# Optimization experiments

Measured on AMD Instinct MI355X. Metric: run time of the kernel, lower is better.

## Reference

```python
import jax, jax.numpy as jnp
import numpy as np

N = 50000      # nodes
E = 800000     # edges (avg degree 16)
F_IN = 256     # input feature dim
H, D = 4, 32   # heads, per-head dim
HD = H * D
K = 25000      # SAGPool keeps ceil(0.5*N) nodes
C = 2          # classes
SLOPE = 0.4
NEG = -1e9

def _gat(x, src, dst, valid, n, W, b, al, ar):
    # DGL GATConv: fc -> per-head attn logits -> edge softmax over dst -> weighted sum
    h = (x @ W).reshape(-1, H, D)                      # [n,H,D]
    el = jnp.einsum('nhd,hd->nh', h, al)
    er = jnp.einsum('nhd,hd->nh', h, ar)
    e = jax.nn.leaky_relu(el[src] + er[dst], SLOPE)    # [E,H]
    e = jnp.where(valid[:, None], e, NEG)
    m = jnp.maximum(jax.ops.segment_max(e, dst, num_segments=n), NEG)
    ex = jnp.exp(e - m[dst]) * valid[:, None].astype(x.dtype)
    s = jax.ops.segment_sum(ex, dst, num_segments=n)
    alpha = ex / jnp.maximum(s[dst], 1e-16)            # [E,H] edge softmax
    out = jax.ops.segment_sum(alpha[:, :, None] * h[src], dst, num_segments=n)
    return out + b.reshape(1, H, D), alpha

def _sagpool(x, src, dst, valid, n, k, Wc, bc):
    # score = GraphConv(in,1) with symmetric norm; keep top-k nodes, scale by tanh(score)
    vf = valid.astype(x.dtype)
    deg_o = jnp.maximum(jax.ops.segment_sum(vf, src, num_segments=n), 1.0)
    deg_i = jnp.maximum(jax.ops.segment_sum(vf, dst, num_segments=n), 1.0)
    h = (x @ Wc) * (deg_o ** -0.5)[:, None]
    agg = jax.ops.segment_sum(h[src] * vf[:, None], dst, num_segments=n)
    score = (agg * (deg_i ** -0.5)[:, None] + bc)[:, 0]   # [n]
    vals, perm = jax.lax.top_k(score, k)
    xk = x[perm] * jnp.tanh(vals)[:, None]                # [k,F]
    new_id = jnp.full((n,), -1, jnp.int32).at[perm].set(jnp.arange(k, dtype=jnp.int32))
    ns, nd = new_id[src], new_id[dst]
    nv = valid & (ns >= 0) & (nd >= 0)                    # edges fully inside subgraph
    return xk, jnp.where(nv, ns, 0), jnp.where(nv, nd, 0), nv

def setup_inputs():
    key = jax.random.key(0)
    k = jax.random.split(key, 18)
    rn = lambda i, shape, scale: jax.random.normal(k[i], shape, jnp.float32) * scale
    return {
        "feature": rn(0, (N, F_IN), 1.0),
        "strength": jax.random.uniform(k[1], (E,), dtype=jnp.float32),
        "W0": rn(2, (F_IN, HD), F_IN ** -0.5), "b0": jnp.zeros((HD,), jnp.float32),
        "al0": rn(3, (H, D), 0.1), "ar0": rn(4, (H, D), 0.1),
        "Wc0": rn(5, (HD, 1), HD ** -0.5), "bc0": jnp.zeros((1,), jnp.float32),
        "W1": rn(6, (HD, HD), HD ** -0.5), "b1": jnp.zeros((HD,), jnp.float32),
        "al1": rn(7, (H, D), 0.1), "ar1": rn(8, (H, D), 0.1),
        "gate_W": rn(9, (D, 1), D ** -0.5), "gate_b": jnp.zeros((1,), jnp.float32),
        "cls_W": rn(10, (D, C), D ** -0.5), "cls_b": jnp.zeros((C,), jnp.float32),
        "src": jax.random.randint(k[11], (E,), 0, N, dtype=jnp.int32),
        "dst": jax.random.randint(k[12], (E,), 0, N, dtype=jnp.int32),
    }

def reference(feature, strength, W0, b0, al0, ar0, Wc0, bc0, W1, b1, al1, ar1,
              gate_W, gate_b, cls_W, cls_b, src, dst):
    valid0 = jnp.ones((E,), bool)
    h0, _ = _gat(feature, src, dst, valid0, N, W0, b0, al0, ar0)
    x = h0.reshape(N, HD)                                  # flatten(1)
    x1, s1, d1, v1 = _sagpool(x, src, dst, valid0, N, K, Wc0, bc0)
    h1, atten = _gat(x1, s1, d1, v1, K, W1, b1, al1, ar1)  # get_attention=True
    strength1 = strength * v1.astype(strength.dtype)       # edata carried into subgraph (masked)
    res = h1.mean(axis=1)                                  # [K,D] mean over heads
    gate = jax.nn.softmax(res @ gate_W + gate_b, axis=0)   # [K,1] GlobalAttentionPooling
    readout = jnp.sum(gate * res, axis=0, keepdims=True)   # [1,D]
    lbl_pred = readout @ cls_W + cls_b                     # [1,C]
    return (readout, lbl_pred, atten, strength1)
```

## Files before the change

### kernel.cpp

```cpp
#include <hip/hip_runtime.h>
#include <stdint.h>

#define NN 50000
#define EE 800000
#define FIN 256
#define HD 128
#define DD 32
#define KK 25000
#define SLOPEF 0.4f
#define NEGF (-1e9f)
#define ATT_OFF 34
#define STR_OFF (34 + EE * 4)
#define CW 128

#define BCH 32
#define EPC (EE / BCH)

__device__ __forceinline__ unsigned fkey(float x) {
    unsigned u = __float_as_uint(x);
    return (u & 0x80000000u) ? ~u : (u | 0x80000000u);
}
__device__ __forceinline__ float unfkey(unsigned k) {
    unsigned u = (k & 0x80000000u) ? (k ^ 0x80000000u) : ~k;
    return __uint_as_float(u);
}
__device__ __forceinline__ float lrelu(float v) { return v > 0.f ? v : SLOPEF * v; }

struct P {
    const float *feature, *strength, *W0, *b0, *al0, *ar0, *Wc0, *bc0;
    const float *W1, *b1, *al1, *ar1, *gW, *gb, *cW, *cb;
    const int *src, *dst;
    double *Zacc, *racc;
    int *cnt;
    unsigned *gmaxk, *rs;
    unsigned *binsHi, *binsLo;
    unsigned *keys;
    unsigned char *degc_i, *degc_o, *degc1;
    unsigned *cb0, *cb1;
    int *dsum;
    int *ens, *end_;
    int *csr_src, *rank, *off0, *off1, *sel, *slot, *list, *bsum, *boff;
    float *z0, *el0, *er0, *q4, *m0f, *s0f, *b0wc, *hc, *score, *xk, *z1;
    float *el1, *er1, *m1f, *s1f, *res, *g, *tscale;
    float *out;
};

#define BM 128
#define BN 64
#define BK 16
__device__ void gemm_body(
    const float* __restrict__ A, const float* __restrict__ B, float* __restrict__ C,
    int M, int Kd,
    const float* __restrict__ al, const float* __restrict__ ar,
    float* __restrict__ el, float* __restrict__ er,
    const float* __restrict__ Wc, float* __restrict__ q4,
    int bx, int by) {
    __shared__ float As[BK][BM + 4];
    __shared__ float Bs[BK][BN];
    int bm = by * BM, bn = bx * BN;
    int tid = threadIdx.x;
    int tr = tid >> 4, tc = tid & 15;
    int lrow = tid >> 1;
    int arow = (bm + lrow < M) ? (bm + lrow) : -1;
    float acc[8][4] = {};
    for (int k0 = 0; k0 < Kd; k0 += BK) {
        {
            int col = (tid & 1) << 3;
            float4 v0 = {0.f,0.f,0.f,0.f}, v1 = {0.f,0.f,0.f,0.f};
            if (arow >= 0) {
                const float* ap = A + (size_t)arow * Kd + k0 + col;
                v0 = *(const float4*)ap; v1 = *(const float4*)(ap + 4);
            }
            As[col + 0][lrow] = v0.x; As[col + 1][lrow] = v0.y;
            As[col + 2][lrow] = v0.z; As[col + 3][lrow] = v0.w;
            As[col + 4][lrow] = v1.x; As[col + 5][lrow] = v1.y;
            As[col + 6][lrow] = v1.z; As[col + 7][lrow] = v1.w;
        }
        {
            int kr = tid >> 4, col = (tid & 15) << 2;
            float4 v = *(const float4*)(B + (size_t)(k0 + kr) * HD + bn + col);
            *(float4*)&Bs[kr][col] = v;
        }
        __syncthreads();
#pragma unroll
        for (int kk = 0; kk < BK; kk++) {
            float a[8], b[4];
#pragma unroll
            for (int i = 0; i < 8; i++) a[i] = As[kk][tr * 8 + i];
#pragma unroll
            for (int j = 0; j < 4; j++) b[j] = Bs[kk][tc * 4 + j];
#pragma unroll
            for (int i = 0; i < 8; i++)
#pragma unroll
                for (int j = 0; j < 4; j++) acc[i][j] = fmaf(a[i], b[j], acc[i][j]);
        }
        __syncthreads();
    }
#pragma unroll
    for (int i = 0; i < 8; i++) {
        int gr = bm + tr * 8 + i;
        if (gr < M) {
            float4 v = {acc[i][0], acc[i][1], acc[i][2], acc[i][3]};
            *(float4*)(C + (size_t)gr * HD + bn + tc * 4) = v;
        }
    }
    int head = bx * 2 + (tc >> 3);
    int dbase = (tc & 7) * 4;
    const float* alh = al + head * 32 + dbase;
    const float* arh = ar + head * 32 + dbase;
    float a0 = alh[0], a1 = alh[1], a2 = alh[2], a3 = alh[3];
    float r0 = arh[0], r1 = arh[1], r2 = arh[2], r3 = arh[3];
    float w0 = 0.f, w1 = 0.f, w2 = 0.f, w3 = 0.f;
    if (Wc) {
        const float* wch = Wc + head * 32 + dbase;
        w0 = wch[0]; w1 = wch[1]; w2 = wch[2]; w3 = wch[3];
    }
#pragma unroll
    for (int i = 0; i < 8; i++) {
        int gr = bm + tr * 8 + i;
        float pe = acc[i][0]*a0 + acc[i][1]*a1 + acc[i][2]*a2 + acc[i][3]*a3;
        float pr = acc[i][0]*r0 + acc[i][1]*r1 + acc[i][2]*r2 + acc[i][3]*r3;
        float pq = acc[i][0]*w0 + acc[i][1]*w1 + acc[i][2]*w2 + acc[i][3]*w3;
#pragma unroll
        for (int o = 1; o < 8; o <<= 1) {
            pe += __shfl_xor(pe, o); pr += __shfl_xor(pr, o); pq += __shfl_xor(pq, o);
        }
        if ((tc & 7) == 0 && gr < M) {
            el[gr * 4 + head] = pe; er[gr * 4 + head] = pr;
            if (Wc) q4[gr * 4 + head] = pq;
        }
    }
}

__global__ __launch_bounds__(256) void k_count0(P p) {
    __shared__ unsigned hist[NN / 4];
    int blk = blockIdx.x;
    int isD = blk < BCH;
    int c = isD ? blk : blk - BCH;
    for (int w = threadIdx.x; w < NN / 4; w += 256) hist[w] = 0u;
    __syncthreads();
    int j0 = c * EPC, j1 = j0 + EPC;
    if (isD) {
        for (int e = j0 + (int)threadIdx.x; e < j1; e += 256) {
            int d = p.dst[e];
            unsigned sh = (unsigned)(d & 3) * 8u;
            unsigned old = atomicAdd(&hist[d >> 2], 1u << sh);
            p.rank[e] = (int)((old >> sh) & 0xffu);
        }
    } else {
        for (int e = j0 + (int)threadIdx.x; e < j1; e += 256) {
            int s = p.src[e];
            atomicAdd(&hist[s >> 2], 1u << ((unsigned)(s & 3) * 8u));
        }
    }
    __syncthreads();
    unsigned* o32 = (unsigned*)((isD ? p.degc_i : p.degc_o) + (size_t)c * NN);
    for (int w = threadIdx.x; w < NN / 4; w += 256) o32[w] = hist[w];
}

__global__ __launch_bounds__(256) void k_count1(P p) {
    __shared__ unsigned hist[KK / 4];
    int c = blockIdx.x;
    for (int w = threadIdx.x; w < KK / 4; w += 256) hist[w] = 0u;
    __syncthreads();
    int j0 = c * EPC, j1 = j0 + EPC;
    for (int e = j0 + (int)threadIdx.x; e < j1; e += 256) {
        int d = p.end_[e];
        if (d >= 0) {
            unsigned sh = (unsigned)(d & 3) * 8u;
            unsigned old = atomicAdd(&hist[d >> 2], 1u << sh);
            p.rank[e] = (int)((old >> sh) & 0xffu);
        }
    }
    __syncthreads();
    unsigned* o32 = (unsigned*)(p.degc1 + (size_t)c * KK);
    for (int w = threadIdx.x; w < KK / 4; w += 256) o32[w] = hist[w];
}

__global__ void k_emap(P p) {
    int e = blockIdx.x * blockDim.x + threadIdx.x;
    if (e >= EE) return;
    int ns = p.slot[p.src[e]], nd = p.slot[p.dst[e]];
    if (ns < 0) nd = -1;
    p.ens[e] = ns;
    p.end_[e] = nd;
}

__global__ __launch_bounds__(256) void k_bsum(const unsigned char* __restrict__ deg,
                                              int* __restrict__ bsum, int n, int nn) {
    int i = blockIdx.x * 256 + threadIdx.x;
    int v = 0;
    if (i < n) {
#pragma unroll
        for (int c = 0; c < BCH; c++) v += deg[(size_t)c * nn + i];
    }
    int lane = threadIdx.x & 63, w = threadIdx.x >> 6;
    __shared__ int ws[4];
#pragma unroll
    for (int o = 1; o < 64; o <<= 1) v += __shfl_xor(v, o);
    if (lane == 0) ws[w] = v;
    __syncthreads();
    if (threadIdx.x == 0) bsum[blockIdx.x] = ws[0] + ws[1] + ws[2] + ws[3];
}
__global__ __launch_bounds__(256) void k_bscan(const int* __restrict__ bsum, int nb,
                                               int* __restrict__ boff,
                                               int* __restrict__ off, int n) {
    __shared__ int ws[4];
    __shared__ int wo[5];
    int t = threadIdx.x;
    int v = (t < nb) ? bsum[t] : 0;
    int lane = t & 63, w = t >> 6;
    int incl = v;
    for (int o = 1; o < 64; o <<= 1) { int u = __shfl_up(incl, o); if (lane >= o) incl += u; }
    if (lane == 63) ws[w] = incl;
    __syncthreads();
    if (t == 0) { int a = 0; for (int i = 0; i < 4; i++) { wo[i] = a; a += ws[i]; } wo[4] = a; }
    __syncthreads();
    if (t < nb) boff[t] = wo[w] + incl - v;
    if (t == 0) off[n] = wo[4];
}
__global__ __launch_bounds__(256) void k_fscan0(P p) {
    __shared__ int ws[4];
    __shared__ int wo[4];
    int i = blockIdx.x * 256 + threadIdx.x;
    int v = 0;
    if (i < NN) {
#pragma unroll
        for (int c = 0; c < BCH; c++) v += p.degc_i[(size_t)c * NN + i];
    }
    int lane = threadIdx.x & 63, w = threadIdx.x >> 6;
    int incl = v;
    for (int o = 1; o < 64; o <<= 1) { int u = __shfl_up(incl, o); if (lane >= o) incl += u; }
    if (lane == 63) ws[w] = incl;
    __syncthreads();
    if (threadIdx.x == 0) { int a = 0; for (int k = 0; k < 4; k++) { wo[k] = a; a += ws[k]; } }
    __syncthreads();
    if (i < NN) {
        int base = p.boff[blockIdx.x] + wo[w] + incl - v;
        p.off0[i] = base;
        unsigned run = (unsigned)base;
        int s = 0;
#pragma unroll
        for (int c = 0; c < BCH; c++) {
            p.cb0[(size_t)c * NN + i] = run;
            run += p.degc_i[(size_t)c * NN + i];
            s += p.degc_o[(size_t)c * NN + i];
        }
        p.dsum[i] = s;
    }
}
__global__ __launch_bounds__(256) void k_fscan1(P p) {
    __shared__ int ws[4];
    __shared__ int wo[4];
    int i = blockIdx.x * 256 + threadIdx.x;
    int v = 0;
    if (i < KK) {
#pragma unroll
        for (int c = 0; c < BCH; c++) v += p.degc1[(size_t)c * KK + i];
    }
    int lane = threadIdx.x & 63, w = threadIdx.x >> 6;
    int incl = v;
    for (int o = 1; o < 64; o <<= 1) { int u = __shfl_up(incl, o); if (lane >= o) incl += u; }
    if (lane == 63) ws[w] = incl;
    __syncthreads();
    if (threadIdx.x == 0) { int a = 0; for (int k = 0; k < 4; k++) { wo[k] = a; a += ws[k]; } }
    __syncthreads();
    if (i < KK) {
        int base = p.boff[blockIdx.x] + wo[w] + incl - v;
        p.off1[i] = base;
        unsigned run = (unsigned)base;
#pragma unroll
        for (int c = 0; c < BCH; c++) {
            p.cb1[(size_t)c * KK + i] = run;
            run += p.degc1[(size_t)c * KK + i];
        }
    }
}

#define G0B 782
#define GB_E 3125
__global__ __launch_bounds__(256) void k_g0sc(P p) {
    int blk = blockIdx.x;
    if (blk < G0B) {
        gemm_body(p.feature, p.W0, p.z0, NN, FIN, p.al0, p.ar0, p.el0, p.er0,
                  p.Wc0, p.q4, blk & 1, blk >> 1);
    } else if (blk < G0B + GB_E) {
        int e = (blk - G0B) * 256 + threadIdx.x;
        if (e < EE) {
            int c = e / EPC;
            int d = p.dst[e];
            unsigned pos = p.cb0[(size_t)c * NN + d] + (unsigned)p.rank[e];
            p.csr_src[pos] = p.src[e];
        }
    } else {
        int l = threadIdx.x;
        if (l < 64) {
            float t = p.b0[l] * p.Wc0[l] + p.b0[l + 64] * p.Wc0[l + 64];
#pragma unroll
            for (int o = 1; o < 64; o <<= 1) t += __shfl_xor(t, o);
            if (l == 0) p.b0wc[0] = t;
        }
    }
}

#define G1B 392
__global__ __launch_bounds__(256) void k_g1sc(P p) {
    int blk = blockIdx.x;
    if (blk < G1B) {
        gemm_body(p.xk, p.W1, p.z1, KK, HD, p.al1, p.ar1, p.el1, p.er1,
                  nullptr, nullptr, blk & 1, blk >> 1);
    } else {
        int e = (blk - G1B) * 256 + threadIdx.x;
        if (e < EE) {
            int d = p.end_[e];
            if (d >= 0) {
                int c = e / EPC;
                unsigned pos = p.cb1[(size_t)c * KK + d] + (unsigned)p.rank[e];
                p.csr_src[pos] = p.ens[e];
            }
        }
    }
}

__global__ __launch_bounds__(256) void k_fgatlite(
    const int* __restrict__ off, const int* __restrict__ csrs,
    const float* __restrict__ el, const float* __restrict__ er,
    const float* __restrict__ q4, const int* __restrict__ dsum,
    const float* __restrict__ b0wc,
    float* __restrict__ hc, float* __restrict__ m0f, float* __restrict__ s0f) {
    int wv = threadIdx.x >> 6, lane = threadIdx.x & 63;
    int v = blockIdx.x * 4 + wv;
    int b = off[v], e = off[v + 1], deg = e - b;
    int h = lane >> 4, sub = lane & 15;
    float erh = er[(size_t)v * 4 + h];
    float m = NEGF;
    for (int li = sub; li < deg; li += 16) {
        int s = csrs[b + li];
        m = fmaxf(m, lrelu(el[(size_t)s * 4 + h] + erh));
    }
#pragma unroll
    for (int o = 1; o < 16; o <<= 1) m = fmaxf(m, __shfl_xor(m, o));
    float ssum = 0.f, hq = 0.f;
    for (int li = sub; li < deg; li += 16) {
        int s = csrs[b + li];
        float ex = expf(lrelu(el[(size_t)s * 4 + h] + erh) - m);
        ssum += ex;
        hq = fmaf(ex, q4[(size_t)s * 4 + h], hq);
    }
#pragma unroll
    for (int o = 1; o < 16; o <<= 1) { ssum += __shfl_xor(ssum, o); hq += __shfl_xor(hq, o); }
    if (sub == 0) { m0f[v * 4 + h] = m; s0f[v * 4 + h] = ssum; }
    float t = hq / fmaxf(ssum, 1e-16f);
    t += __shfl_xor(t, 16);
    t += __shfl_xor(t, 32);
    if (lane == 0)
        hc[v] = (t + b0wc[0]) / sqrtf(fmaxf((float)dsum[v], 1.f));
}

__global__ __launch_bounds__(256) void k_fgatx(
    const int* __restrict__ list, const float* __restrict__ tscale,
    const int* __restrict__ off, const int* __restrict__ csrs,
    const float* __restrict__ el, const float* __restrict__ er,
    const float* __restrict__ m0f, const float* __restrict__ s0f,
    const float* __restrict__ z, const float* __restrict__ b0,
    float* __restrict__ xk) {
    __shared__ int ssrc[4][CW];
    __shared__ float sexp[4][CW][4];
    int wv = threadIdx.x >> 6, lane = threadIdx.x & 63;
    int i = blockIdx.x * 4 + wv;
    int v = list[i];
    int b = off[v], e = off[v + 1], deg = e - b;
    int h = lane >> 4, sub = lane & 15;
    float erh = er[(size_t)v * 4 + h];
    float mh = m0f[v * 4 + h];
    for (int li = sub; li < deg; li += 16) {
        int s = csrs[b + li];
        if (h == 0 && li < CW) ssrc[wv][li] = s;
        if (li < CW) sexp[wv][li][h] = expf(lrelu(el[(size_t)s * 4 + h] + erh) - mh);
    }
    __syncthreads();
    int h0 = lane >> 5, h1 = h0 + 2;
    float s0 = s0f[v * 4 + h0], s1 = s0f[v * 4 + h1];
    float m0 = m0f[v * 4 + h0], m1 = m0f[v * 4 + h1];
    float er0v = er[(size_t)v * 4 + h0], er1v = er[(size_t)v * 4 + h1];
    int c0 = lane, c1 = lane + 64;
    float acc0 = 0.f, acc1 = 0.f;
    for (int li = 0; li < deg; li++) {
        int s; float w0, w1;
        if (li < CW) {
            s = ssrc[wv][li];
            w0 = sexp[wv][li][h0]; w1 = sexp[wv][li][h1];
        } else {
            s = csrs[b + li];
            w0 = expf(lrelu(el[(size_t)s * 4 + h0] + er0v) - m0);
            w1 = expf(lrelu(el[(size_t)s * 4 + h1] + er1v) - m1);
        }
        int su = __builtin_amdgcn_readfirstlane(s);
        const float* zr = z + (size_t)su * HD;
        acc0 = fmaf(w0, zr[c0], acc0);
        acc1 = fmaf(w1, zr[c1], acc1);
    }
    float ts = tscale[i];
    float* xr = xk + (size_t)i * HD;
    xr[c0] = (acc0 / fmaxf(s0, 1e-16f) + b0[c0]) * ts;
    xr[c1] = (acc1 / fmaxf(s1, 1e-16f) + b0[c1]) * ts;
}

__global__ void k_score(P p) {
    int v = blockIdx.x * blockDim.x + threadIdx.x;
    if (v >= NN) return;
    int b = p.off0[v], en = p.off0[v + 1];
    float acc = 0.f;
    for (int i = b; i < en; i++) acc += p.hc[p.csr_src[i]];
    float dg = fmaxf((float)(en - b), 1.f);
    float sc = acc / sqrtf(dg) + p.bc0[0];
    p.score[v] = sc;
    p.keys[v] = fkey(sc);
}

__global__ void k_hist2(P p, int level) {
    int v = blockIdx.x * blockDim.x + threadIdx.x;
    if (v >= NN) return;
    unsigned key = p.keys[v];
    if (level == 0) atomicAdd(&p.binsHi[key >> 16], 1u);
    else if ((key >> 16) == p.rs[2]) atomicAdd(&p.binsLo[key & 0xFFFFu], 1u);
}
__global__ __launch_bounds__(1024) void k_rsel2(P p, int level) {
    const unsigned* bins = level ? p.binsLo : p.binsHi;
    int K = level ? (int)p.rs[3] : KK;
    __shared__ unsigned wsm[16];
    __shared__ unsigned wpre[17];
    int t = threadIdx.x;
    unsigned base = (unsigned)t * 64;
    const uint4* b4 = (const uint4*)(bins + base);
    unsigned S = 0;
#pragma unroll
    for (int i = 0; i < 16; i++) {
        uint4 u = b4[i];
        S += u.x + u.y + u.z + u.w;
    }
    int lane = t & 63, w = t >> 6;
    unsigned val = S;
    for (int o = 1; o < 64; o <<= 1) { unsigned u = __shfl_up(val, o); if (lane >= o) val += u; }
    if (lane == 63) wsm[w] = val;
    __syncthreads();
    if (t == 0) { unsigned a = 0; for (int i = 0; i < 16; i++) { wpre[i] = a; a += wsm[i]; } wpre[16] = a; }
    __syncthreads();
    unsigned incl = wpre[w] + val;
    unsigned running = wpre[16] - incl;
    for (int i = 63; i >= 0; i--) {
        unsigned c = bins[base + i];
        unsigned above = running;
        running += c;
        if ((int)above < K && (int)running >= K) {
            if (level == 0) { p.rs[2] = base + (unsigned)i; p.rs[3] = (unsigned)(K - (int)above); }
            else { p.rs[0] = (p.rs[2] << 16) | (base + (unsigned)i); p.rs[1] = (unsigned)(K - (int)above); }
        }
    }
}
__global__ void k_sel(P p) {
    int v = blockIdx.x * blockDim.x + threadIdx.x;
    if (v >= NN) return;
    p.sel[v] = (p.keys[v] > p.rs[0]) ? 1 : 0;
}
__global__ __launch_bounds__(1024) void k_ties(P p) {
    __shared__ int base;
    __shared__ int wsums[16];
    unsigned pivot = p.rs[0];
    int need = (int)p.rs[1];
    if (threadIdx.x == 0) base = 0;
    __syncthreads();
    for (int st = 0; st < NN; st += 1024) {
        int v = st + (int)threadIdx.x;
        int flag = (v < NN && p.keys[v] == pivot) ? 1 : 0;
        unsigned long long m = __ballot(flag);
        int lane = threadIdx.x & 63, w = threadIdx.x >> 6;
        int pre = __popcll(m & ((1ull << lane) - 1ull));
        if (lane == 0) wsums[w] = __popcll(m);
        __syncthreads();
        int woff = 0;
        for (int i = 0; i < w; i++) woff += wsums[i];
        int rank = base + woff + pre;
        if (flag && rank < need) p.sel[v] = 1;
        __syncthreads();
        if (threadIdx.x == 0) {
            int s = 0;
            for (int i = 0; i < 16; i++) s += wsums[i];
            base += s;
        }
        __syncthreads();
    }
}
__global__ void k_list(P p) {
    int v = blockIdx.x * blockDim.x + threadIdx.x;
    if (v >= NN) return;
    if (p.sel[v]) {
        int i = atomicAdd(p.cnt, 1);
        p.list[i] = v;
        p.slot[v] = i;
        p.tscale[i] = tanhf(p.score[v]);
    } else {
        p.slot[v] = -1;
    }
}

__global__ __launch_bounds__(256) void k_fgat2(
    const int* __restrict__ off, const int* __restrict__ csrs,
    const float* __restrict__ el, const float* __restrict__ er,
    const float* __restrict__ z, const float* __restrict__ bias,
    float* __restrict__ mf, float* __restrict__ sf,
    const float* __restrict__ gW, const float* __restrict__ gb,
    float* __restrict__ res, float* __restrict__ g) {
    __shared__ int ssrc[4][CW];
    __shared__ float sexp[4][CW][4];
    int wv = threadIdx.x >> 6, lane = threadIdx.x & 63;
    int v = blockIdx.x * 4 + wv;
    int b = off[v], e = off[v + 1], deg = e - b;
    int h = lane >> 4, sub = lane & 15;
    float4 er4 = *(const float4*)(er + (size_t)v * 4);
    float erh = ((const float*)&er4)[h];
    float m = NEGF;
    for (int li = sub; li < deg; li += 16) {
        int s = csrs[b + li];
        if (h == 0 && li < CW) ssrc[wv][li] = s;
        m = fmaxf(m, lrelu(el[(size_t)s * 4 + h] + erh));
    }
#pragma unroll
    for (int o = 1; o < 16; o <<= 1) m = fmaxf(m, __shfl_xor(m, o));
    float ssum = 0.f;
    for (int li = sub; li < deg; li += 16) {
        int s = csrs[b + li];
        float x = expf(lrelu(el[(size_t)s * 4 + h] + erh) - m);
        if (li < CW) sexp[wv][li][h] = x;
        ssum += x;
    }
#pragma unroll
    for (int o = 1; o < 16; o <<= 1) ssum += __shfl_xor(ssum, o);
    if (sub == 0) { mf[v * 4 + h] = m; sf[v * 4 + h] = ssum; }
    __syncthreads();
    int h0 = lane >> 5, h1 = h0 + 2;
    float m0 = __shfl(m, h0 << 4), m1 = __shfl(m, h1 << 4);
    float s0 = __shfl(ssum, h0 << 4), s1 = __shfl(ssum, h1 << 4);
    int c0 = lane, c1 = lane + 64;
    float acc0 = 0.f, acc1 = 0.f;
    for (int li = 0; li < deg; li++) {
        int s; float w0, w1;
        if (li < CW) {
            s = ssrc[wv][li];
            w0 = sexp[wv][li][h0]; w1 = sexp[wv][li][h1];
        } else {
            s = csrs[b + li];
            w0 = expf(lrelu(el[(size_t)s * 4 + h0] + ((const float*)&er4)[h0]) - m0);
            w1 = expf(lrelu(el[(size_t)s * 4 + h1] + ((const float*)&er4)[h1]) - m1);
        }
        int su = __builtin_amdgcn_readfirstlane(s);
        const float* zr = z + (size_t)su * HD;
        acc0 = fmaf(w0, zr[c0], acc0);
        acc1 = fmaf(w1, zr[c1], acc1);
    }
    float xc0 = acc0 / fmaxf(s0, 1e-16f) + bias[c0];
    float xc1 = acc1 / fmaxf(s1, 1e-16f) + bias[c1];
    float t = xc0 + xc1;
    t += __shfl_xor(t, 32);
    float pg = 0.f;
    if (lane < 32) {
        float r = 0.25f * t;
        res[(size_t)v * 32 + lane] = r;
        pg = r * gW[lane];
    }
#pragma unroll
    for (int o = 1; o < 32; o <<= 1) pg += __shfl_xor(pg, o);
    if (lane == 0) g[v] = pg + gb[0];
}

__global__ void k_ealpha1(P p) {
    int e = blockIdx.x * blockDim.x + threadIdx.x;
    if (e >= EE) return;
    int ds = p.ens[e], dd = p.end_[e];
    float a[4] = {0.f, 0.f, 0.f, 0.f};
    float st = 0.f;
    if (dd >= 0) {
        float4 es = *(const float4*)(p.el1 + ds * 4);
        float4 ed = *(const float4*)(p.er1 + dd * 4);
        float l[4] = {lrelu(es.x + ed.x), lrelu(es.y + ed.y), lrelu(es.z + ed.z), lrelu(es.w + ed.w)};
#pragma unroll
        for (int h = 0; h < 4; h++) {
            float m = p.m1f[dd * 4 + h];
            float ex = expf(l[h] - m);
            a[h] = ex / fmaxf(p.s1f[dd * 4 + h], 1e-16f);
        }
        st = p.strength[e];
    }
    float* o = p.out + ATT_OFF + (size_t)e * 4;
    *(float2*)(o) = make_float2(a[0], a[1]);
    *(float2*)(o + 2) = make_float2(a[2], a[3]);
    p.out[STR_OFF + e] = st;
}

__global__ void k_gmax(P p) {
    __shared__ float red[256];
    int t = threadIdx.x;
    float m = -3.4e38f;
    for (int i = blockIdx.x * 256 + t; i < KK; i += gridDim.x * 256) m = fmaxf(m, p.g[i]);
    red[t] = m;
    __syncthreads();
    for (int o = 128; o > 0; o >>= 1) { if (t < o) red[t] = fmaxf(red[t], red[t + o]); __syncthreads(); }
    if (t == 0) atomicMax(p.gmaxk, fkey(red[0]));
}
#define WSUM_BLOCKS 104
__global__ __launch_bounds__(256) void k_wsum(P p) {
    __shared__ double vred[256];
    __shared__ double zred[8];
    int t = threadIdx.x, il = t >> 5, d = t & 31;
    float gm = unfkey(*p.gmaxk);
    double accv = 0.0, accw = 0.0;
    for (int i = blockIdx.x * 8 + il; i < KK; i += WSUM_BLOCKS * 8) {
        float w = expf(p.g[i] - gm);
        accv += (double)(w * p.res[(size_t)i * 32 + d]);
        if (d == 0) accw += (double)w;
    }
    vred[t] = accv;
    if (d == 0) zred[il] = accw;
    __syncthreads();
    if (il == 0) {
        double s = 0;
#pragma unroll
        for (int k2 = 0; k2 < 8; k2++) s += vred[k2 * 32 + d];
        atomicAdd(&p.racc[d], s);
    }
    if (t == 32) {
        double z2 = 0;
#pragma unroll
        for (int k2 = 0; k2 < 8; k2++) z2 += zred[k2];
        atomicAdd(p.Zacc, z2);
    }
}
__global__ void k_final(P p) {
    __shared__ float rb[32];
    int t = threadIdx.x;
    double Z = *p.Zacc;
    if (t < 32) {
        float r = (float)(p.racc[t] / Z);
        p.out[t] = r;
        rb[t] = r;
    }
    __syncthreads();
    if (t < 2) {
        float s = 0.f;
        for (int d = 0; d < 32; d++) s += rb[d] * p.cW[d * 2 + t];
        p.out[32 + t] = s + p.cb[t];
    }
}

extern "C" void kernel_launch(void* const* d_in, const int* in_sizes, int n_in,
                              void* d_out, int out_size, void* d_ws, size_t ws_size,
                              hipStream_t stream) {
    (void)in_sizes; (void)n_in; (void)out_size; (void)ws_size;
    P p;
    p.feature  = (const float*)d_in[0];
    p.strength = (const float*)d_in[1];
    p.W0  = (const float*)d_in[2];  p.b0  = (const float*)d_in[3];
    p.al0 = (const float*)d_in[4];  p.ar0 = (const float*)d_in[5];
    p.Wc0 = (const float*)d_in[6];  p.bc0 = (const float*)d_in[7];
    p.W1  = (const float*)d_in[8];  p.b1  = (const float*)d_in[9];
    p.al1 = (const float*)d_in[10]; p.ar1 = (const float*)d_in[11];
    p.gW  = (const float*)d_in[12]; p.gb  = (const float*)d_in[13];
    p.cW  = (const float*)d_in[14]; p.cb  = (const float*)d_in[15];
    p.src = (const int*)d_in[16];   p.dst = (const int*)d_in[17];
    p.out = (float*)d_out;

    char* ws = (char*)d_ws;
    size_t off = 0;
    auto alloc = [&](size_t bytes) -> void* {
        void* r = ws + off;
        off = (off + bytes + 255) & ~(size_t)255;
        return r;
    };
    p.Zacc  = (double*)alloc(8);
    p.racc  = (double*)alloc(32 * 8);
    p.cnt   = (int*)alloc(4);
    p.gmaxk = (unsigned*)alloc(4);
    p.rs    = (unsigned*)alloc(16);
    p.binsHi = (unsigned*)alloc(65536 * 4);
    p.binsLo = (unsigned*)alloc(65536 * 4);
    size_t zbytes = off;
    p.degc_i = (unsigned char*)alloc((size_t)BCH * NN);
    p.degc_o = (unsigned char*)alloc((size_t)BCH * NN);
    p.degc1  = p.degc_i;
    p.cb0 = (unsigned*)alloc((size_t)BCH * NN * 4);
    p.cb1 = p.cb0;
    p.dsum = (int*)alloc((size_t)NN * 4);
    p.ens  = (int*)alloc((size_t)EE * 4);
    p.end_ = (int*)alloc((size_t)EE * 4);
    p.z0 = (float*)alloc((size_t)NN * HD * 4);
    p.xk = (float*)alloc((size_t)KK * HD * 4);
    p.z1 = (float*)alloc((size_t)KK * HD * 4);
    p.csr_src = (int*)alloc((size_t)EE * 4);
    p.rank    = (int*)alloc((size_t)EE * 4);
    p.el0 = (float*)alloc((size_t)NN * 4 * 4);
    p.er0 = (float*)alloc((size_t)NN * 4 * 4);
    p.q4  = (float*)alloc((size_t)NN * 4 * 4);
    p.m0f = (float*)alloc((size_t)NN * 4 * 4);
    p.s0f = (float*)alloc((size_t)NN * 4 * 4);
    p.b0wc = (float*)alloc(4);
    p.off0 = (int*)alloc((size_t)(NN + 1) * 4);
    p.off1 = (int*)alloc((size_t)(KK + 1) * 4);
    p.bsum = (int*)alloc(256 * 4);
    p.boff = (int*)alloc(256 * 4);
    p.hc    = (float*)alloc((size_t)NN * 4);
    p.score = (float*)alloc((size_t)NN * 4);
    p.keys  = (unsigned*)alloc((size_t)NN * 4);
    p.sel   = (int*)alloc((size_t)NN * 4);
    p.slot  = (int*)alloc((size_t)NN * 4);
    p.list  = (int*)alloc((size_t)KK * 4);
    p.tscale = (float*)alloc((size_t)KK * 4);
    p.el1 = (float*)alloc((size_t)KK * 4 * 4);
    p.er1 = (float*)alloc((size_t)KK * 4 * 4);
    p.m1f = (float*)alloc((size_t)KK * 4 * 4);
    p.s1f = (float*)alloc((size_t)KK * 4 * 4);
    p.res = (float*)alloc((size_t)KK * DD * 4);
    p.g   = (float*)alloc((size_t)KK * 4);

    const int GB_N = (NN + 255) / 256;
    const int GB_K = (KK + 255) / 256;

    hipMemsetAsync(d_ws, 0, zbytes, stream);

    k_count0<<<2 * BCH, 256, 0, stream>>>(p);
    k_bsum<<<GB_N, 256, 0, stream>>>(p.degc_i, p.bsum, NN, NN);
    k_bscan<<<1, 256, 0, stream>>>(p.bsum, GB_N, p.boff, p.off0, NN);
    k_fscan0<<<GB_N, 256, 0, stream>>>(p);
    k_g0sc<<<G0B + GB_E + 1, 256, 0, stream>>>(p);
    k_fgatlite<<<NN / 4, 256, 0, stream>>>(p.off0, p.csr_src, p.el0, p.er0, p.q4,
                                           p.dsum, p.b0wc, p.hc, p.m0f, p.s0f);

    k_score<<<GB_N, 256, 0, stream>>>(p);
    k_hist2<<<GB_N, 256, 0, stream>>>(p, 0);
    k_rsel2<<<1, 1024, 0, stream>>>(p, 0);
    k_hist2<<<GB_N, 256, 0, stream>>>(p, 1);
    k_rsel2<<<1, 1024, 0, stream>>>(p, 1);
    k_sel<<<GB_N, 256, 0, stream>>>(p);
    k_ties<<<1, 1024, 0, stream>>>(p);
    k_list<<<GB_N, 256, 0, stream>>>(p);

    k_emap<<<GB_E, 256, 0, stream>>>(p);
    k_count1<<<BCH, 256, 0, stream>>>(p);
    k_bsum<<<GB_K, 256, 0, stream>>>(p.degc1, p.bsum, KK, KK);
    k_bscan<<<1, 256, 0, stream>>>(p.bsum, GB_K, p.boff, p.off1, KK);
    k_fscan1<<<GB_K, 256, 0, stream>>>(p);
    k_fgatx<<<KK / 4, 256, 0, stream>>>(p.list, p.tscale, p.off0, p.csr_src,
                                        p.el0, p.er0, p.m0f, p.s0f, p.z0, p.b0, p.xk);
    k_g1sc<<<G1B + GB_E, 256, 0, stream>>>(p);
    k_fgat2<<<KK / 4, 256, 0, stream>>>(p.off1, p.csr_src, p.el1, p.er1, p.z1, p.b1,
                                        p.m1f, p.s1f, p.gW, p.gb, p.res, p.g);
    k_ealpha1<<<GB_E, 256, 0, stream>>>(p);

    k_gmax<<<98, 256, 0, stream>>>(p);
    k_wsum<<<WSUM_BLOCKS, 256, 0, stream>>>(p);
    k_final<<<1, 64, 0, stream>>>(p);
}
```

Baseline: 630.0 us.

## Reuse layer-0 CSR for pooled GAT and block-privatize top-k histograms

Drops the separate subgraph CSR build (edge remap, counting, scan and scatter kernels). The second GAT now walks the original layer-0 CSR and filters neighbors through the slot map. The top-k radix histograms move to shared-memory privatized 16-bit packed counters in 1024-thread blocks, replacing per-element global atomics. Score storage and the separate sel kernel are folded into k_score and k_list. This removes several launches and edge-sized passes, at the cost of visiting non-selected neighbors and doing extra slot lookups in the second aggregation.

Result: faster. 579.7 us (-8.0%).

```diff
diff --git a/kernel.cpp b/kernel.cpp
--- a/kernel.cpp
+++ b/kernel.cpp
@@ -32,15 +32,15 @@
     const int *src, *dst;
     double *Zacc, *racc;
     int *cnt;
-    unsigned *gmaxk, *rs;
+    unsigned *gmaxk;
+    unsigned *rs;
     unsigned *binsHi, *binsLo;
     unsigned *keys;
-    unsigned char *degc_i, *degc_o, *degc1;
-    unsigned *cb0, *cb1;
+    unsigned char *degc_i, *degc_o;
+    unsigned *cb0;
     int *dsum;
-    int *ens, *end_;
-    int *csr_src, *rank, *off0, *off1, *sel, *slot, *list, *bsum, *boff;
-    float *z0, *el0, *er0, *q4, *m0f, *s0f, *b0wc, *hc, *score, *xk, *z1;
+    int *csr_src, *rank, *off0, *sel, *slot, *list, *bsum, *boff;
+    float *z0, *el0, *er0, *q4, *m0f, *s0f, *b0wc, *hc, *xk, *z1;
     float *el1, *er1, *m1f, *s1f, *res, *g, *tscale;
     float *out;
 };
@@ -158,34 +158,6 @@
     for (int w = threadIdx.x; w < NN / 4; w += 256) o32[w] = hist[w];
 }
 
-__global__ __launch_bounds__(256) void k_count1(P p) {
-    __shared__ unsigned hist[KK / 4];
-    int c = blockIdx.x;
-    for (int w = threadIdx.x; w < KK / 4; w += 256) hist[w] = 0u;
-    __syncthreads();
-    int j0 = c * EPC, j1 = j0 + EPC;
-    for (int e = j0 + (int)threadIdx.x; e < j1; e += 256) {
-        int d = p.end_[e];
-        if (d >= 0) {
-            unsigned sh = (unsigned)(d & 3) * 8u;
-            unsigned old = atomicAdd(&hist[d >> 2], 1u << sh);
-            p.rank[e] = (int)((old >> sh) & 0xffu);
-        }
-    }
-    __syncthreads();
-    unsigned* o32 = (unsigned*)(p.degc1 + (size_t)c * KK);
-    for (int w = threadIdx.x; w < KK / 4; w += 256) o32[w] = hist[w];
-}
-
-__global__ void k_emap(P p) {
-    int e = blockIdx.x * blockDim.x + threadIdx.x;
-    if (e >= EE) return;
-    int ns = p.slot[p.src[e]], nd = p.slot[p.dst[e]];
-    if (ns < 0) nd = -1;
-    p.ens[e] = ns;
-    p.end_[e] = nd;
-}
-
 __global__ __launch_bounds__(256) void k_bsum(const unsigned char* __restrict__ deg,
                                               int* __restrict__ bsum, int n, int nn) {
     int i = blockIdx.x * 256 + threadIdx.x;
@@ -247,33 +219,6 @@
             s += p.degc_o[(size_t)c * NN + i];
         }
         p.dsum[i] = s;
-    }
-}
-__global__ __launch_bounds__(256) void k_fscan1(P p) {
-    __shared__ int ws[4];
-    __shared__ int wo[4];
-    int i = blockIdx.x * 256 + threadIdx.x;
-    int v = 0;
-    if (i < KK) {
-#pragma unroll
-        for (int c = 0; c < BCH; c++) v += p.degc1[(size_t)c * KK + i];
-    }
-    int lane = threadIdx.x & 63, w = threadIdx.x >> 6;
-    int incl = v;
-    for (int o = 1; o < 64; o <<= 1) { int u = __shfl_up(incl, o); if (lane >= o) incl += u; }
-    if (lane == 63) ws[w] = incl;
-    __syncthreads();
-    if (threadIdx.x == 0) { int a = 0; for (int k = 0; k < 4; k++) { wo[k] = a; a += ws[k]; } }
-    __syncthreads();
-    if (i < KK) {
-        int base = p.boff[blockIdx.x] + wo[w] + incl - v;
-        p.off1[i] = base;
-        unsigned run = (unsigned)base;
-#pragma unroll
-        for (int c = 0; c < BCH; c++) {
-            p.cb1[(size_t)c * KK + i] = run;
-            run += p.degc1[(size_t)c * KK + i];
-        }
     }
 }
 
@@ -299,25 +244,6 @@
 #pragma unroll
             for (int o = 1; o < 64; o <<= 1) t += __shfl_xor(t, o);
             if (l == 0) p.b0wc[0] = t;
-        }
-    }
-}
-
-#define G1B 392
-__global__ __launch_bounds__(256) void k_g1sc(P p) {
-    int blk = blockIdx.x;
-    if (blk < G1B) {
-        gemm_body(p.xk, p.W1, p.z1, KK, HD, p.al1, p.ar1, p.el1, p.er1,
-                  nullptr, nullptr, blk & 1, blk >> 1);
-    } else {
-        int e = (blk - G1B) * 256 + threadIdx.x;
-        if (e < EE) {
-            int d = p.end_[e];
-            if (d >= 0) {
-                int c = e / EPC;
-                unsigned pos = p.cb1[(size_t)c * KK + d] + (unsigned)p.rank[e];
-                p.csr_src[pos] = p.ens[e];
-            }
         }
     }
 }
@@ -355,6 +281,147 @@
     t += __shfl_xor(t, 32);
     if (lane == 0)
         hc[v] = (t + b0wc[0]) / sqrtf(fmaxf((float)dsum[v], 1.f));
+}
+
+__global__ __launch_bounds__(256) void k_score(P p) {
+    int v = blockIdx.x * blockDim.x + threadIdx.x;
+    if (v >= NN) return;
+    int b = p.off0[v], en = p.off0[v + 1];
+    float acc = 0.f;
+    for (int i = b; i < en; i++) acc += p.hc[p.csr_src[i]];
+    float dg = fmaxf((float)(en - b), 1.f);
+    float sc = acc / sqrtf(dg) + p.bc0[0];
+    p.keys[v] = fkey(sc);
+    p.sel[v] = 0;
+}
+
+#define HB 49
+__global__ __launch_bounds__(1024) void k_h0(P p) {
+    __shared__ unsigned hist[16384];
+    int i = blockIdx.x * 1024 + (int)threadIdx.x;
+    unsigned key = (i < NN) ? p.keys[i] : 0xFFFFFFFFu;
+    unsigned b16 = key >> 16;
+#pragma unroll
+    for (int half = 0; half < 2; half++) {
+        for (int w = threadIdx.x; w < 16384; w += 1024) hist[w] = 0u;
+        __syncthreads();
+        if (i < NN && (int)(b16 >> 15) == half) {
+            unsigned bb = b16 & 0x7FFFu;
+            atomicAdd(&hist[bb >> 1], 1u << (16u * (bb & 1u)));
+        }
+        __syncthreads();
+        for (int w = threadIdx.x; w < 16384; w += 1024) {
+            unsigned hv = hist[w];
+            unsigned lo = hv & 0xFFFFu, hi = hv >> 16;
+            if (lo) atomicAdd(&p.binsHi[half * 32768 + 2 * w], lo);
+            if (hi) atomicAdd(&p.binsHi[half * 32768 + 2 * w + 1], hi);
+        }
+        __syncthreads();
+    }
+}
+
+__global__ __launch_bounds__(1024) void k_h1(P p) {
+    __shared__ unsigned hist[16384];
+    int i = blockIdx.x * 1024 + (int)threadIdx.x;
+    unsigned hib = p.rs[2];
+    unsigned key = (i < NN) ? p.keys[i] : 0u;
+    int cand = (i < NN) && ((key >> 16) == hib);
+    unsigned b16 = key & 0xFFFFu;
+#pragma unroll
+    for (int half = 0; half < 2; half++) {
+        for (int w = threadIdx.x; w < 16384; w += 1024) hist[w] = 0u;
+        __syncthreads();
+        if (cand && (int)(b16 >> 15) == half) {
+            unsigned bb = b16 & 0x7FFFu;
+            atomicAdd(&hist[bb >> 1], 1u << (16u * (bb & 1u)));
+        }
+        __syncthreads();
+        for (int w = threadIdx.x; w < 16384; w += 1024) {
+            unsigned hv = hist[w];
+            unsigned lo = hv & 0xFFFFu, hi = hv >> 16;
+            if (lo) atomicAdd(&p.binsLo[half * 32768 + 2 * w], lo);
+            if (hi) atomicAdd(&p.binsLo[half * 32768 + 2 * w + 1], hi);
+        }
+        __syncthreads();
+    }
+}
+
+__global__ __launch_bounds__(1024) void k_rsel2(P p, int level) {
+    const unsigned* bins = level ? p.binsLo : p.binsHi;
+    int K = level ? (int)p.rs[3] : KK;
+    __shared__ unsigned wsm[16];
+    __shared__ unsigned wpre[17];
+    int t = threadIdx.x;
+    unsigned base = (unsigned)t * 64;
+    const uint4* b4 = (const uint4*)(bins + base);
+    unsigned S = 0;
+#pragma unroll
+    for (int i = 0; i < 16; i++) {
+        uint4 u = b4[i];
+        S += u.x + u.y + u.z + u.w;
+    }
+    int lane = t & 63, w = t >> 6;
+    unsigned val = S;
+    for (int o = 1; o < 64; o <<= 1) { unsigned u = __shfl_up(val, o); if (lane >= o) val += u; }
+    if (lane == 63) wsm[w] = val;
+    __syncthreads();
+    if (t == 0) { unsigned a = 0; for (int i = 0; i < 16; i++) { wpre[i] = a; a += wsm[i]; } wpre[16] = a; }
+    __syncthreads();
+    unsigned incl = wpre[w] + val;
+    unsigned running = wpre[16] - incl;
+    for (int i = 63; i >= 0; i--) {
+        unsigned c = bins[base + i];
+        unsigned above = running;
+        running += c;
+        if ((int)above < K && (int)running >= K) {
+            if (level == 0) { p.rs[2] = base + (unsigned)i; p.rs[3] = (unsigned)(K - (int)above); }
+            else { p.rs[0] = (p.rs[2] << 16) | (base + (unsigned)i); p.rs[1] = (unsigned)(K - (int)above); }
+        }
+    }
+}
+
+__global__ __launch_bounds__(1024) void k_ties(P p) {
+    __shared__ int base;
+    __shared__ int wsums[16];
+    unsigned pivot = p.rs[0];
+    int need = (int)p.rs[1];
+    if (threadIdx.x == 0) base = 0;
+    __syncthreads();
+    for (int st = 0; st < NN; st += 1024) {
+        int v = st + (int)threadIdx.x;
+        int flag = (v < NN && p.keys[v] == pivot) ? 1 : 0;
+        unsigned long long m = __ballot(flag);
+        int lane = threadIdx.x & 63, w = threadIdx.x >> 6;
+        int pre = __popcll(m & ((1ull << lane) - 1ull));
+        if (lane == 0) wsums[w] = __popcll(m);
+        __syncthreads();
+        int woff = 0;
+        for (int i = 0; i < w; i++) woff += wsums[i];
+        int rank = base + woff + pre;
+        if (flag && rank < need) p.sel[v] = 1;
+        __syncthreads();
+        if (threadIdx.x == 0) {
+            int s = 0;
+            for (int i = 0; i < 16; i++) s += wsums[i];
+            base += s;
+        }
+        __syncthreads();
+    }
+}
+
+__global__ void k_list(P p) {
+    int v = blockIdx.x * blockDim.x + threadIdx.x;
+    if (v >= NN) return;
+    unsigned k = p.keys[v];
+    int selv = (k > p.rs[0]) || p.sel[v];
+    if (selv) {
+        int i = atomicAdd(p.cnt, 1);
+        p.list[i] = v;
+        p.slot[v] = i;
+        p.tscale[i] = tanhf(unfkey(k));
+    } else {
+        p.slot[v] = -1;
+    }
 }
 
 __global__ __launch_bounds__(256) void k_fgatx(
@@ -406,137 +473,42 @@
     xr[c1] = (acc1 / fmaxf(s1, 1e-16f) + b0[c1]) * ts;
 }
 
-__global__ void k_score(P p) {
-    int v = blockIdx.x * blockDim.x + threadIdx.x;
-    if (v >= NN) return;
-    int b = p.off0[v], en = p.off0[v + 1];
-    float acc = 0.f;
-    for (int i = b; i < en; i++) acc += p.hc[p.csr_src[i]];
-    float dg = fmaxf((float)(en - b), 1.f);
-    float sc = acc / sqrtf(dg) + p.bc0[0];
-    p.score[v] = sc;
-    p.keys[v] = fkey(sc);
-}
-
-__global__ void k_hist2(P p, int level) {
-    int v = blockIdx.x * blockDim.x + threadIdx.x;
-    if (v >= NN) return;
-    unsigned key = p.keys[v];
-    if (level == 0) atomicAdd(&p.binsHi[key >> 16], 1u);
-    else if ((key >> 16) == p.rs[2]) atomicAdd(&p.binsLo[key & 0xFFFFu], 1u);
-}
-__global__ __launch_bounds__(1024) void k_rsel2(P p, int level) {
-    const unsigned* bins = level ? p.binsLo : p.binsHi;
-    int K = level ? (int)p.rs[3] : KK;
-    __shared__ unsigned wsm[16];
-    __shared__ unsigned wpre[17];
-    int t = threadIdx.x;
-    unsigned base = (unsigned)t * 64;
-    const uint4* b4 = (const uint4*)(bins + base);
-    unsigned S = 0;
-#pragma unroll
-    for (int i = 0; i < 16; i++) {
-        uint4 u = b4[i];
-        S += u.x + u.y + u.z + u.w;
-    }
-    int lane = t & 63, w = t >> 6;
-    unsigned val = S;
-    for (int o = 1; o < 64; o <<= 1) { unsigned u = __shfl_up(val, o); if (lane >= o) val += u; }
-    if (lane == 63) wsm[w] = val;
-    __syncthreads();
-    if (t == 0) { unsigned a = 0; for (int i = 0; i < 16; i++) { wpre[i] = a; a += wsm[i]; } wpre[16] = a; }
-    __syncthreads();
-    unsigned incl = wpre[w] + val;
-    unsigned running = wpre[16] - incl;
-    for (int i = 63; i >= 0; i--) {
-        unsigned c = bins[base + i];
-        unsigned above = running;
-        running += c;
-        if ((int)above < K && (int)running >= K) {
-            if (level == 0) { p.rs[2] = base + (unsigned)i; p.rs[3] = (unsigned)(K - (int)above); }
-            else { p.rs[0] = (p.rs[2] << 16) | (base + (unsigned)i); p.rs[1] = (unsigned)(K - (int)above); }
-        }
-    }
-}
-__global__ void k_sel(P p) {
-    int v = blockIdx.x * blockDim.x + threadIdx.x;
-    if (v >= NN) return;
-    p.sel[v] = (p.keys[v] > p.rs[0]) ? 1 : 0;
-}
-__global__ __launch_bounds__(1024) void k_ties(P p) {
-    __shared__ int base;
-    __shared__ int wsums[16];
-    unsigned pivot = p.rs[0];
-    int need = (int)p.rs[1];
-    if (threadIdx.x == 0) base = 0;
-    __syncthreads();
-    for (int st = 0; st < NN; st += 1024) {
-        int v = st + (int)threadIdx.x;
-        int flag = (v < NN && p.keys[v] == pivot) ? 1 : 0;
-        unsigned long long m = __ballot(flag);
-        int lane = threadIdx.x & 63, w = threadIdx.x >> 6;
-        int pre = __popcll(m & ((1ull << lane) - 1ull));
-        if (lane == 0) wsums[w] = __popcll(m);
-        __syncthreads();
-        int woff = 0;
-        for (int i = 0; i < w; i++) woff += wsums[i];
-        int rank = base + woff + pre;
-        if (flag && rank < need) p.sel[v] = 1;
-        __syncthreads();
-        if (threadIdx.x == 0) {
-            int s = 0;
-            for (int i = 0; i < 16; i++) s += wsums[i];
-            base += s;
-        }
-        __syncthreads();
-    }
-}
-__global__ void k_list(P p) {
-    int v = blockIdx.x * blockDim.x + threadIdx.x;
-    if (v >= NN) return;
-    if (p.sel[v]) {
-        int i = atomicAdd(p.cnt, 1);
-        p.list[i] = v;
-        p.slot[v] = i;
-        p.tscale[i] = tanhf(p.score[v]);
-    } else {
-        p.slot[v] = -1;
-    }
-}
-
-__global__ __launch_bounds__(256) void k_fgat2(
-    const int* __restrict__ off, const int* __restrict__ csrs,
-    const float* __restrict__ el, const float* __restrict__ er,
-    const float* __restrict__ z, const float* __restrict__ bias,
-    float* __restrict__ mf, float* __restrict__ sf,
-    const float* __restrict__ gW, const float* __restrict__ gb,
-    float* __restrict__ res, float* __restrict__ g) {
+#define G1B 392
+__global__ __launch_bounds__(256) void k_gemm1(P p) {
+    gemm_body(p.xk, p.W1, p.z1, KK, HD, p.al1, p.ar1, p.el1, p.er1,
+              nullptr, nullptr, blockIdx.x & 1, blockIdx.x >> 1);
+}
+
+__global__ __launch_bounds__(256) void k_fgat2(P p) {
     __shared__ int ssrc[4][CW];
     __shared__ float sexp[4][CW][4];
     int wv = threadIdx.x >> 6, lane = threadIdx.x & 63;
-    int v = blockIdx.x * 4 + wv;
-    int b = off[v], e = off[v + 1], deg = e - b;
+    int i = blockIdx.x * 4 + wv;
+    int v = p.list[i];
+    int b = p.off0[v], e = p.off0[v + 1], deg = e - b;
     int h = lane >> 4, sub = lane & 15;
-    float4 er4 = *(const float4*)(er + (size_t)v * 4);
+    float4 er4 = *(const float4*)(p.er1 + (size_t)i * 4);
     float erh = ((const float*)&er4)[h];
     float m = NEGF;
     for (int li = sub; li < deg; li += 16) {
-        int s = csrs[b + li];
-        if (h == 0 && li < CW) ssrc[wv][li] = s;
-        m = fmaxf(m, lrelu(el[(size_t)s * 4 + h] + erh));
+        int so = p.csr_src[b + li];
+        int ss = p.slot[so];
+        if (h == 0 && li < CW) ssrc[wv][li] = ss;
+        if (ss >= 0) m = fmaxf(m, lrelu(p.el1[(size_t)ss * 4 + h] + erh));
     }
 #pragma unroll
     for (int o = 1; o < 16; o <<= 1) m = fmaxf(m, __shfl_xor(m, o));
     float ssum = 0.f;
     for (int li = sub; li < deg; li += 16) {
-        int s = csrs[b + li];
-        float x = expf(lrelu(el[(size_t)s * 4 + h] + erh) - m);
+        int so = p.csr_src[b + li];
+        int ss = p.slot[so];
+        float x = (ss >= 0) ? expf(lrelu(p.el1[(size_t)ss * 4 + h] + erh) - m) : 0.f;
         if (li < CW) sexp[wv][li][h] = x;
         ssum += x;
     }
 #pragma unroll
     for (int o = 1; o < 16; o <<= 1) ssum += __shfl_xor(ssum, o);
-    if (sub == 0) { mf[v * 4 + h] = m; sf[v * 4 + h] = ssum; }
+    if (sub == 0) { p.m1f[i * 4 + h] = m; p.s1f[i * 4 + h] = ssum; }
     __syncthreads();
     int h0 = lane >> 5, h1 = h0 + 2;
     float m0 = __shfl(m, h0 << 4), m1 = __shfl(m, h1 << 4);
@@ -547,39 +519,42 @@
         int s; float w0, w1;
         if (li < CW) {
             s = ssrc[wv][li];
+            if (s < 0) continue;
             w0 = sexp[wv][li][h0]; w1 = sexp[wv][li][h1];
         } else {
-            s = csrs[b + li];
-            w0 = expf(lrelu(el[(size_t)s * 4 + h0] + ((const float*)&er4)[h0]) - m0);
-            w1 = expf(lrelu(el[(size_t)s * 4 + h1] + ((const float*)&er4)[h1]) - m1);
+            int so = p.csr_src[b + li];
+            s = p.slot[so];
+            if (s < 0) continue;
+            w0 = expf(lrelu(p.el1[(size_t)s * 4 + h0] + ((const float*)&er4)[h0]) - m0);
+            w1 = expf(lrelu(p.el1[(size_t)s * 4 + h1] + ((const float*)&er4)[h1]) - m1);
         }
         int su = __builtin_amdgcn_readfirstlane(s);
-        const float* zr = z + (size_t)su * HD;
+        const float* zr = p.z1 + (size_t)su * HD;
         acc0 = fmaf(w0, zr[c0], acc0);
         acc1 = fmaf(w1, zr[c1], acc1);
     }
-    float xc0 = acc0 / fmaxf(s0, 1e-16f) + bias[c0];
-    float xc1 = acc1 / fmaxf(s1, 1e-16f) + bias[c1];
+    float xc0 = acc0 / fmaxf(s0, 1e-16f) + p.b1[c0];
+    float xc1 = acc1 / fmaxf(s1, 1e-16f) + p.b1[c1];
     float t = xc0 + xc1;
     t += __shfl_xor(t, 32);
     float pg = 0.f;
     if (lane < 32) {
         float r = 0.25f * t;
-        res[(size_t)v * 32 + lane] = r;
-        pg = r * gW[lane];
+        p.res[(size_t)i * 32 + lane] = r;
+        pg = r * p.gW[lane];
     }
 #pragma unroll
     for (int o = 1; o < 32; o <<= 1) pg += __shfl_xor(pg, o);
-    if (lane == 0) g[v] = pg + gb[0];
+    if (lane == 0) p.g[i] = pg + p.gb[0];
 }
 
 __global__ void k_ealpha1(P p) {
     int e = blockIdx.x * blockDim.x + threadIdx.x;
     if (e >= EE) return;
-    int ds = p.ens[e], dd = p.end_[e];
+    int ds = p.slot[p.src[e]], dd = p.slot[p.dst[e]];
     float a[4] = {0.f, 0.f, 0.f, 0.f};
     float st = 0.f;
-    if (dd >= 0) {
+    if (ds >= 0 && dd >= 0) {
         float4 es = *(const float4*)(p.el1 + ds * 4);
         float4 ed = *(const float4*)(p.er1 + dd * 4);
         float l[4] = {lrelu(es.x + ed.x), lrelu(es.y + ed.y), lrelu(es.z + ed.z), lrelu(es.w + ed.w)};
@@ -686,12 +661,8 @@
     size_t zbytes = off;
     p.degc_i = (unsigned char*)alloc((size_t)BCH * NN);
     p.degc_o = (unsigned char*)alloc((size_t)BCH * NN);
-    p.degc1  = p.degc_i;
     p.cb0 = (unsigned*)alloc((size_t)BCH * NN * 4);
-    p.cb1 = p.cb0;
     p.dsum = (int*)alloc((size_t)NN * 4);
-    p.ens  = (int*)alloc((size_t)EE * 4);
-    p.end_ = (int*)alloc((size_t)EE * 4);
     p.z0 = (float*)alloc((size_t)NN * HD * 4);
     p.xk = (float*)alloc((size_t)KK * HD * 4);
     p.z1 = (float*)alloc((size_t)KK * HD * 4);
@@ -704,11 +675,9 @@
     p.s0f = (float*)alloc((size_t)NN * 4 * 4);
     p.b0wc = (float*)alloc(4);
     p.off0 = (int*)alloc((size_t)(NN + 1) * 4);
-    p.off1 = (int*)alloc((size_t)(KK + 1) * 4);
     p.bsum = (int*)alloc(256 * 4);
     p.boff = (int*)alloc(256 * 4);
     p.hc    = (float*)alloc((size_t)NN * 4);
-    p.score = (float*)alloc((size_t)NN * 4);
     p.keys  = (unsigned*)alloc((size_t)NN * 4);
     p.sel   = (int*)alloc((size_t)NN * 4);
     p.slot  = (int*)alloc((size_t)NN * 4);
@@ -722,7 +691,6 @@
     p.g   = (float*)alloc((size_t)KK * 4);
 
     const int GB_N = (NN + 255) / 256;
-    const int GB_K = (KK + 255) / 256;
 
     hipMemsetAsync(d_ws, 0, zbytes, stream);
 
@@ -735,24 +703,17 @@
                                            p.dsum, p.b0wc, p.hc, p.m0f, p.s0f);
 
     k_score<<<GB_N, 256, 0, stream>>>(p);
-    k_hist2<<<GB_N, 256, 0, stream>>>(p, 0);
+    k_h0<<<HB, 1024, 0, stream>>>(p);
     k_rsel2<<<1, 1024, 0, stream>>>(p, 0);
-    k_hist2<<<GB_N, 256, 0, stream>>>(p, 1);
+    k_h1<<<HB, 1024, 0, stream>>>(p);
     k_rsel2<<<1, 1024, 0, stream>>>(p, 1);
-    k_sel<<<GB_N, 256, 0, stream>>>(p);
     k_ties<<<1, 1024, 0, stream>>>(p);
     k_list<<<GB_N, 256, 0, stream>>>(p);
 
-    k_emap<<<GB_E, 256, 0, stream>>>(p);
-    k_count1<<<BCH, 256, 0, stream>>>(p);
-    k_bsum<<<GB_K, 256, 0, stream>>>(p.degc1, p.bsum, KK, KK);
-    k_bscan<<<1, 256, 0, stream>>>(p.bsum, GB_K, p.boff, p.off1, KK);
-    k_fscan1<<<GB_K, 256, 0, stream>>>(p);
     k_fgatx<<<KK / 4, 256, 0, stream>>>(p.list, p.tscale, p.off0, p.csr_src,
                                         p.el0, p.er0, p.m0f, p.s0f, p.z0, p.b0, p.xk);
-    k_g1sc<<<G1B + GB_E, 256, 0, stream>>>(p);
-    k_fgat2<<<KK / 4, 256, 0, stream>>>(p.off1, p.csr_src, p.el1, p.er1, p.z1, p.b1,
-                                        p.m1f, p.s1f, p.gW, p.gb, p.res, p.g);
+    k_gemm1<<<G1B, 256, 0, stream>>>(p);
+    k_fgat2<<<KK / 4, 256, 0, stream>>>(p);
     k_ealpha1<<<GB_E, 256, 0, stream>>>(p);
 
     k_gmax<<<98, 256, 0, stream>>>(p);
```
